# Performance work log

Hardware: AMD Instinct MI355X
Metric: run time of the kernel (lower is better)

## Reference

```python
import jax, jax.numpy as jnp
import numpy as np

N, L, C = 2, 1024, 256
H, E, CL, LAYERS = 64, 16, 64, 4


def setup_inputs() -> dict:
    key = jax.random.key(0)
    ks = jax.random.split(key, 12)
    s = 0.05
    return {
        "x": jax.random.normal(ks[0], (N, L, C), jnp.float32),
        "Wq": jax.random.normal(ks[1], (H * E, C), jnp.float32) * s,
        "bq": jax.random.normal(ks[2], (H * E,), jnp.float32) * s,
        "Wk": jax.random.normal(ks[3], (H * E, C), jnp.float32) * s,
        "bk": jax.random.normal(ks[4], (H * E,), jnp.float32) * s,
        "Wv": jax.random.normal(ks[5], (H, C), jnp.float32) * s,
        "bv": jax.random.normal(ks[6], (H,), jnp.float32) * s,
        "PE": jax.random.uniform(ks[7], (CL, H, E), jnp.float32),
        "fc_w": jax.random.normal(ks[8], (LAYERS, H, H), jnp.float32) * s,
        "fc_b": jax.random.normal(ks[9], (LAYERS, H), jnp.float32) * s,
        "Wout": jax.random.normal(ks[10], (3, H), jnp.float32) * s,
        "bout": jax.random.normal(ks[11], (3,), jnp.float32) * s,
    }


def reference(x, Wq, bq, Wk, bk, Wv, bv, PE, fc_w, fc_b, Wout, bout):
    n, l, c = x.shape
    cl, h, e_dim = PE.shape
    q = (x @ Wq.T + bq).reshape(n, l, h, e_dim)   # (N,L,H,E)
    k = (x @ Wk.T + bk).reshape(n, l, h, e_dim)   # (N,L,H,E)
    v = x @ Wv.T + bv                             # (N,L,H)
    # sliding-window offsets: row i gathers positions i..i+cl-1
    off = jnp.arange(l - cl)[:, None] + jnp.arange(cl)[None, :]  # (L-cl, cl)
    q_mid = q[:, cl // 2: l - cl // 2]            # (N,L-cl,H,E) center queries
    k_win = k[:, off]                             # (N,L-cl,cl,H,E) gathered keys
    # e_{h,id} = q.k + q.PE  (distributed instead of adding PE to k_win)
    e = (jnp.einsum('nlhe,nldhe->nldh', q_mid, k_win)
         + jnp.einsum('nlhe,dhe->nldh', q_mid, PE))
    a = jax.nn.softmax(e, axis=2)                 # softmax over window offset d
    v_win = v[:, off]                             # (N,L-cl,cl,H)
    out = jnp.einsum('nldh,nldh->nlh', a, v_win)  # weighted sum over d
    out = jax.nn.relu(out)
    for i in range(fc_w.shape[0]):                # 1x1 Conv1d stack == per-pos linear
        out = jax.nn.relu(jnp.einsum('nlh,oh->nlo', out, fc_w[i]) + fc_b[i])
    out = jnp.einsum('nlh,oh->nlo', out, Wout) + bout  # (N,L-cl,3)
    return out
```

## Files before the change

### kernel.cpp

```cpp
#include <hip/hip_runtime.h>


typedef __attribute__((ext_vector_type(8))) __bf16 bf16x8;
typedef __attribute__((ext_vector_type(8))) short short8;
typedef __attribute__((ext_vector_type(4))) float f32x4;

__device__ inline unsigned short bf16_rne(float x) {
    unsigned u = __builtin_bit_cast(unsigned, x);
    unsigned r = u + 0x7fffu + ((u >> 16) & 1u);
    return (unsigned short)(r >> 16);
}
__device__ inline float bf16_f(unsigned short h) {
    return __builtin_bit_cast(float, (unsigned)h << 16);
}

__global__ __launch_bounds__(256) void convert_split(
    const float* __restrict__ X,
    const float* __restrict__ Wq, const float* __restrict__ Wk, const float* __restrict__ Wv,
    unsigned short* __restrict__ XhG, unsigned short* __restrict__ XlG,
    unsigned short* __restrict__ WhG, unsigned short* __restrict__ WlG)
{
    const int g = blockIdx.x * 256 + threadIdx.x;
    const int NX = 131072;
    const int NW = 135168;
    if (g >= NX + NW) return;

    float4 v;
    unsigned short *dh, *dl;
    int off;
    if (g < NX) {
        off = g * 4;
        v = *reinterpret_cast<const float4*>(&X[off]);
        dh = XhG; dl = XlG;
    } else {
        off = (g - NX) * 4;
        const int row = off >> 8, col = off & 255;
        const float* s;
        if (row < 1024)      s = &Wq[row * 256 + col];
        else if (row < 2048) s = &Wk[(row - 1024) * 256 + col];
        else                 s = &Wv[(row - 2048) * 256 + col];
        v = *reinterpret_cast<const float4*>(s);
        dh = WhG; dl = WlG;
    }
    unsigned short h0 = bf16_rne(v.x), h1 = bf16_rne(v.y), h2 = bf16_rne(v.z), h3 = bf16_rne(v.w);
    unsigned short l0 = bf16_rne(v.x - bf16_f(h0));
    unsigned short l1 = bf16_rne(v.y - bf16_f(h1));
    unsigned short l2 = bf16_rne(v.z - bf16_f(h2));
    unsigned short l3 = bf16_rne(v.w - bf16_f(h3));
    ushort4 hv = make_ushort4(h0, h1, h2, h3);
    ushort4 lv = make_ushort4(l0, l1, l2, l3);
    *reinterpret_cast<ushort4*>(&dh[off]) = hv;
    *reinterpret_cast<ushort4*>(&dl[off]) = lv;
}

#define LDA 72

__global__ __launch_bounds__(256) void qkv_mfma(
    const unsigned short* __restrict__ XhG, const unsigned short* __restrict__ XlG,
    const unsigned short* __restrict__ WhG, const unsigned short* __restrict__ WlG,
    const float* __restrict__ bq, const float* __restrict__ bk, const float* __restrict__ bv,
    float* __restrict__ qT, float* __restrict__ kT, float* __restrict__ vT)
{
    __shared__ unsigned short A_lds[128 * LDA];
    __shared__ unsigned short B_lds[128 * LDA];
    __shared__ unsigned short C_lds[128 * LDA];

    const int tid = threadIdx.x;
    const int lane = tid & 63;
    const int wid = tid >> 6;
    const int wm = wid >> 1, wn = wid & 1;
    const int m0 = blockIdx.x * 128;
    const int o0 = blockIdx.y * 128;

    f32x4 acc[4][4];
    #pragma unroll
    for (int i = 0; i < 4; ++i)
        #pragma unroll
        for (int j = 0; j < 4; ++j)
            acc[i][j] = f32x4{0.f, 0.f, 0.f, 0.f};

    const short8 zero8 = {0, 0, 0, 0, 0, 0, 0, 0};

    for (int k0 = 0; k0 < 256; k0 += 64) {
        __syncthreads();
        #pragma unroll
        for (int i = tid; i < 1024; i += 256) {
            const int row = i >> 3, lc = (i & 7) * 8;
            *reinterpret_cast<short8*>(&A_lds[row * LDA + lc]) =
                *reinterpret_cast<const short8*>(&XhG[(m0 + row) * 256 + k0 + lc]);
            const int orow = o0 + row;
            short8 wh = zero8, wl = zero8;
            if (orow < 2112) {
                wh = *reinterpret_cast<const short8*>(&WhG[orow * 256 + k0 + lc]);
                wl = *reinterpret_cast<const short8*>(&WlG[orow * 256 + k0 + lc]);
            }
            *reinterpret_cast<short8*>(&B_lds[row * LDA + lc]) = wh;
            *reinterpret_cast<short8*>(&C_lds[row * LDA + lc]) = wl;
        }
        __syncthreads();
        #pragma unroll
        for (int kk = 0; kk < 64; kk += 32) {
            const int colb = kk + ((lane >> 4) << 3);
            bf16x8 aH[4], bH[4], bL[4];
            #pragma unroll
            for (int t = 0; t < 4; ++t) {
                const int ar = wm * 64 + t * 16 + (lane & 15);
                const int br = wn * 64 + t * 16 + (lane & 15);
                aH[t] = __builtin_bit_cast(bf16x8, *reinterpret_cast<const short8*>(&A_lds[ar * LDA + colb]));
                bH[t] = __builtin_bit_cast(bf16x8, *reinterpret_cast<const short8*>(&B_lds[br * LDA + colb]));
                bL[t] = __builtin_bit_cast(bf16x8, *reinterpret_cast<const short8*>(&C_lds[br * LDA + colb]));
            }
            #pragma unroll
            for (int mt = 0; mt < 4; ++mt)
                #pragma unroll
                for (int ot = 0; ot < 4; ++ot) {
                    acc[mt][ot] = __builtin_amdgcn_mfma_f32_16x16x32_bf16(aH[mt], bH[ot], acc[mt][ot], 0, 0, 0);
                    acc[mt][ot] = __builtin_amdgcn_mfma_f32_16x16x32_bf16(aH[mt], bL[ot], acc[mt][ot], 0, 0, 0);
                }
        }
        __syncthreads();
        #pragma unroll
        for (int i = tid; i < 1024; i += 256) {
            const int row = i >> 3, lc = (i & 7) * 8;
            *reinterpret_cast<short8*>(&C_lds[row * LDA + lc]) =
                *reinterpret_cast<const short8*>(&XlG[(m0 + row) * 256 + k0 + lc]);
        }
        __syncthreads();
        #pragma unroll
        for (int kk = 0; kk < 64; kk += 32) {
            const int colb = kk + ((lane >> 4) << 3);
            bf16x8 aL[4], bH[4];
            #pragma unroll
            for (int t = 0; t < 4; ++t) {
                const int ar = wm * 64 + t * 16 + (lane & 15);
                const int br = wn * 64 + t * 16 + (lane & 15);
                aL[t] = __builtin_bit_cast(bf16x8, *reinterpret_cast<const short8*>(&C_lds[ar * LDA + colb]));
                bH[t] = __builtin_bit_cast(bf16x8, *reinterpret_cast<const short8*>(&B_lds[br * LDA + colb]));
            }
            #pragma unroll
            for (int mt = 0; mt < 4; ++mt)
                #pragma unroll
                for (int ot = 0; ot < 4; ++ot)
                    acc[mt][ot] = __builtin_amdgcn_mfma_f32_16x16x32_bf16(aL[mt], bH[ot], acc[mt][ot], 0, 0, 0);
        }
    }

    const int drow = (lane >> 4) * 4;
    const int dcol = lane & 15;
    const int mode = (o0 < 1024) ? 0 : (o0 < 2048 ? 1 : 2);

    if (mode < 2) {
        float* __restrict__ T = mode ? kT : qT;
        const float* __restrict__ bias = mode ? bk : bq;
        const int ob = mode * 1024;
        #pragma unroll
        for (int ot = 0; ot < 4; ++ot) {
            const int o = o0 + wn * 64 + ot * 16 + dcol;
            const int h = (o >> 4) & 63;
            const int e = o & 15;
            const float bval = bias[o - ob];
            #pragma unroll
            for (int mt = 0; mt < 4; ++mt)
                #pragma unroll
                for (int r = 0; r < 4; ++r) {
                    const int m = m0 + wm * 64 + mt * 16 + drow + r;
                    const int n = m >> 10, l = m & 1023;
                    T[((n * 64 + h) * 1024 + l) * 16 + e] = acc[mt][ot][r] + bval;
                }
        }
    } else if (wn == 0) {
        #pragma unroll
        for (int ot = 0; ot < 4; ++ot) {
            const int hV = ot * 16 + dcol;
            const float bval = bv[hV];
            #pragma unroll
            for (int mt = 0; mt < 4; ++mt)
                #pragma unroll
                for (int r = 0; r < 4; ++r) {
                    const int m = m0 + wm * 64 + mt * 16 + drow + r;
                    const int n = m >> 10, l = m & 1023;
                    vT[(n * 64 + hV) * 1024 + l] = acc[mt][ot][r] + bval;
                }
        }
    }
}

__global__ __launch_bounds__(64) void attn_kernel(
    const float* __restrict__ qT, const float* __restrict__ kT,
    const float* __restrict__ vT, const float* __restrict__ PE,
    float* __restrict__ attT)
{
    __shared__ float k_lds[127 * 20];
    __shared__ float pe_lds[64 * 16];
    __shared__ float v_lds[128];

    const int lane = threadIdx.x;
    const int lt = blockIdx.x;
    const int h  = blockIdx.y;
    const int n  = blockIdx.z;
    const int l0 = lt * 64;

    const float4* kb4 = reinterpret_cast<const float4*>(kT + ((size_t)(n * 64 + h) * 1024 + l0) * 16);
    for (int u = lane; u < 508; u += 64) {
        float4 g = kb4[u];
        const int row = u >> 2, f = u & 3;
        *reinterpret_cast<float4*>(&k_lds[row * 20 + f * 4]) = g;
    }
    for (int u = lane; u < 256; u += 64) {
        const int d = u >> 2, f = u & 3;
        *reinterpret_cast<float4*>(&pe_lds[d * 16 + f * 4]) =
            *reinterpret_cast<const float4*>(&PE[(d * 64 + h) * 16 + f * 4]);
    }
    const float* vbase = vT + (size_t)(n * 64 + h) * 1024 + l0;
    for (int u = lane; u < 127; u += 64) v_lds[u] = vbase[u];

    float4 q0, q1, q2, q3;
    {
        const float4* qb = reinterpret_cast<const float4*>(
            qT + ((size_t)(n * 64 + h) * 1024 + l0 + 32 + lane) * 16);
        q0 = qb[0]; q1 = qb[1]; q2 = qb[2]; q3 = qb[3];
    }
    __syncthreads();

    float den = 0.f, pv = 0.f;
    #pragma unroll 2
    for (int d = 0; d < 64; ++d) {
        const float4* kr = reinterpret_cast<const float4*>(&k_lds[(lane + d) * 20]);
        const float4* pr = reinterpret_cast<const float4*>(&pe_lds[d * 16]);
        const float4 k0 = kr[0], k1 = kr[1], k2 = kr[2], k3 = kr[3];
        const float4 p0 = pr[0], p1 = pr[1], p2 = pr[2], p3 = pr[3];
        float s0 = (k0.x + p0.x) * q0.x + (k0.y + p0.y) * q0.y
                 + (k0.z + p0.z) * q0.z + (k0.w + p0.w) * q0.w;
        float s1 = (k1.x + p1.x) * q1.x + (k1.y + p1.y) * q1.y
                 + (k1.z + p1.z) * q1.z + (k1.w + p1.w) * q1.w;
        float s2 = (k2.x + p2.x) * q2.x + (k2.y + p2.y) * q2.y
                 + (k2.z + p2.z) * q2.z + (k2.w + p2.w) * q2.w;
        float s3 = (k3.x + p3.x) * q3.x + (k3.y + p3.y) * q3.y
                 + (k3.z + p3.z) * q3.z + (k3.w + p3.w) * q3.w;
        const float s = (s0 + s1) + (s2 + s3);
        const float p = __expf(s - 16.f);
        den += p;
        pv += p * v_lds[lane + d];
    }
    attT[(size_t)(n * 64 + h) * 960 + l0 + lane] = fmaxf(pv / den, 0.f);
}

__global__ __launch_bounds__(256) void fc_kernel(
    const float* __restrict__ attT,
    const float* __restrict__ fc_w, const float* __restrict__ fc_b,
    const float* __restrict__ Wout, const float* __restrict__ bout,
    float* __restrict__ out)
{
    __shared__ float w_lds[64 * 68];
    __shared__ float wo_lds[3 * 64];
    __shared__ float bufA[4 * 68];
    __shared__ float bufB[4 * 68];

    const int tid = threadIdx.x;
    const int o = tid & 63;
    const int r = tid >> 6;
    const int R0 = blockIdx.x * 4;
    const int n = R0 / 960;
    const int l0 = R0 - n * 960;

    for (int idx = tid; idx < 192; idx += 256) wo_lds[idx] = Wout[idx];
    {
        const int hh = tid >> 2, rr = tid & 3;
        bufA[rr * 68 + hh] = attT[(size_t)(n * 64 + hh) * 960 + l0 + rr];
    }

    float* cur = bufA;
    float* nxt = bufB;

    for (int layer = 0; layer < 4; ++layer) {
        __syncthreads();
        const float4* wsrc = reinterpret_cast<const float4*>(fc_w + layer * 4096);
        for (int u = tid; u < 1024; u += 256) {
            const int oo = u >> 4, f = u & 15;
            *reinterpret_cast<float4*>(&w_lds[oo * 68 + f * 4]) = wsrc[u];
        }
        __syncthreads();
        float acc = fc_b[layer * 64 + o];
        const float4* wr = reinterpret_cast<const float4*>(&w_lds[o * 68]);
        const float4* cr = reinterpret_cast<const float4*>(&cur[r * 68]);
        #pragma unroll
        for (int t = 0; t < 16; ++t) {
            const float4 c = cr[t], w = wr[t];
            acc += c.x * w.x + c.y * w.y + c.z * w.z + c.w * w.w;
        }
        nxt[r * 68 + o] = fmaxf(acc, 0.f);
        float* tmp = cur; cur = nxt; nxt = tmp;
    }
    __syncthreads();

    if (o < 3) {
        float acc = bout[o];
        #pragma unroll
        for (int hh = 0; hh < 64; ++hh)
            acc += cur[r * 68 + hh] * wo_lds[o * 64 + hh];
        out[(R0 + r) * 3 + o] = acc;
    }
}

extern "C" void kernel_launch(void* const* d_in, const int* in_sizes, int n_in,
                              void* d_out, int out_size, void* d_ws, size_t ws_size,
                              hipStream_t stream) {
    const float* x    = (const float*)d_in[0];
    const float* Wq   = (const float*)d_in[1];
    const float* bq   = (const float*)d_in[2];
    const float* Wk   = (const float*)d_in[3];
    const float* bk   = (const float*)d_in[4];
    const float* Wv   = (const float*)d_in[5];
    const float* bv   = (const float*)d_in[6];
    const float* PE   = (const float*)d_in[7];
    const float* fc_w = (const float*)d_in[8];
    const float* fc_b = (const float*)d_in[9];
    const float* Wout = (const float*)d_in[10];
    const float* bout = (const float*)d_in[11];
    float* out = (float*)d_out;

    float* ws = (float*)d_ws;
    float* qT   = ws;
    float* kT   = qT + 2097152;
    float* vT   = kT + 2097152;
    float* attT = vT + 131072;
    unsigned short* XhG = (unsigned short*)(attT + 122880);
    unsigned short* XlG = XhG + 524288;
    unsigned short* WhG = XlG + 524288;
    unsigned short* WlG = WhG + 540672;

    convert_split<<<1040, 256, 0, stream>>>(x, Wq, Wk, Wv, XhG, XlG, WhG, WlG);
    qkv_mfma<<<dim3(16, 17), 256, 0, stream>>>(XhG, XlG, WhG, WlG, bq, bk, bv, qT, kT, vT);
    attn_kernel<<<dim3(15, 64, 2), 64, 0, stream>>>(qT, kT, vT, PE, attT);
    fc_kernel<<<480, 256, 0, stream>>>(attT, fc_w, fc_b, Wout, bout, out);
}
```

Before: 62.59 us.

## Stage QKV GEMM tiles via direct global-to-LDS loads with XOR swizzle

Rewrites the QKV split-bf16 GEMM staging. All four operand tiles (X hi/lo, W hi/lo) are loaded in one pass with global_load_lds straight into an XOR-swizzled LDS buffer, replacing register-staged padded copies and the second reload of X-lo. The block grows to 512 threads (8 waves, each 64x32), and the three MFMAs per tile pair run in a single loop. The intent is to cut LDS staging overhead and barriers and raise the number of waves in flight. The row guard on W was removed, so the last column block reads past the weight rows (into WlG and possibly past it), though those outputs are discarded.

After: 53.00 us. 1.18x faster.

```diff
diff --git a/kernel.cpp b/kernel.cpp
--- a/kernel.cpp
+++ b/kernel.cpp
@@ -53,96 +53,82 @@
     *reinterpret_cast<ushort4*>(&dl[off]) = lv;
 }
 
-#define LDA 72
-
-__global__ __launch_bounds__(256) void qkv_mfma(
+__device__ __forceinline__ bf16x8 ldsfrag(const unsigned short* lds, int t, int row, int so) {
+    return __builtin_bit_cast(bf16x8, *reinterpret_cast<const short8*>(
+        lds + t * 8192 + row * 64 + (((so ^ (row & 7)) & 7) << 3)));
+}
+
+__global__ __launch_bounds__(512, 4) void qkv_mfma(
     const unsigned short* __restrict__ XhG, const unsigned short* __restrict__ XlG,
     const unsigned short* __restrict__ WhG, const unsigned short* __restrict__ WlG,
     const float* __restrict__ bq, const float* __restrict__ bk, const float* __restrict__ bv,
     float* __restrict__ qT, float* __restrict__ kT, float* __restrict__ vT)
 {
-    __shared__ unsigned short A_lds[128 * LDA];
-    __shared__ unsigned short B_lds[128 * LDA];
-    __shared__ unsigned short C_lds[128 * LDA];
-
-    const int tid = threadIdx.x;
+    __shared__ unsigned short lds[4 * 128 * 64];
+
+    const int tid  = threadIdx.x;
     const int lane = tid & 63;
-    const int wid = tid >> 6;
-    const int wm = wid >> 1, wn = wid & 1;
+    const int wid  = tid >> 6;
+    const int wm   = wid >> 2;
+    const int wn   = wid & 3;
     const int m0 = blockIdx.x * 128;
     const int o0 = blockIdx.y * 128;
 
-    f32x4 acc[4][4];
+    f32x4 acc[4][2];
     #pragma unroll
     for (int i = 0; i < 4; ++i)
         #pragma unroll
-        for (int j = 0; j < 4; ++j)
+        for (int j = 0; j < 2; ++j)
             acc[i][j] = f32x4{0.f, 0.f, 0.f, 0.f};
 
-    const short8 zero8 = {0, 0, 0, 0, 0, 0, 0, 0};
+    const int r8 = lane >> 3;
+    const int ss = (lane & 7) ^ r8;
 
     for (int k0 = 0; k0 < 256; k0 += 64) {
+        #pragma unroll
+        for (int j = 0; j < 8; ++j) {
+            const int c   = (wid << 3) | j;
+            const int t   = c >> 4;
+            const int rg  = c & 15;
+            const int row = (rg << 3) + r8;
+            const unsigned short* gsrc;
+            if (t == 0)      gsrc = &XhG[(m0 + row) * 256 + k0 + (ss << 3)];
+            else if (t == 1) gsrc = &XlG[(m0 + row) * 256 + k0 + (ss << 3)];
+            else if (t == 2) gsrc = &WhG[(o0 + row) * 256 + k0 + (ss << 3)];
+            else             gsrc = &WlG[(o0 + row) * 256 + k0 + (ss << 3)];
+            char* lbase = (char*)lds + (c << 10);
+            __builtin_amdgcn_global_load_lds(
+                (const __attribute__((address_space(1))) void*)gsrc,
+                (__attribute__((address_space(3))) void*)lbase, 16, 0, 0);
+        }
         __syncthreads();
-        #pragma unroll
-        for (int i = tid; i < 1024; i += 256) {
-            const int row = i >> 3, lc = (i & 7) * 8;
-            *reinterpret_cast<short8*>(&A_lds[row * LDA + lc]) =
-                *reinterpret_cast<const short8*>(&XhG[(m0 + row) * 256 + k0 + lc]);
-            const int orow = o0 + row;
-            short8 wh = zero8, wl = zero8;
-            if (orow < 2112) {
-                wh = *reinterpret_cast<const short8*>(&WhG[orow * 256 + k0 + lc]);
-                wl = *reinterpret_cast<const short8*>(&WlG[orow * 256 + k0 + lc]);
+
+        #pragma unroll
+        for (int kk = 0; kk < 64; kk += 32) {
+            const int so = (kk >> 3) + (lane >> 4);
+            bf16x8 aH[4], aL[4], bH[2], bL[2];
+            #pragma unroll
+            for (int mt = 0; mt < 4; ++mt) {
+                const int ar = wm * 64 + mt * 16 + (lane & 15);
+                aH[mt] = ldsfrag(lds, 0, ar, so);
+                aL[mt] = ldsfrag(lds, 1, ar, so);
             }
-            *reinterpret_cast<short8*>(&B_lds[row * LDA + lc]) = wh;
-            *reinterpret_cast<short8*>(&C_lds[row * LDA + lc]) = wl;
-        }
-        __syncthreads();
-        #pragma unroll
-        for (int kk = 0; kk < 64; kk += 32) {
-            const int colb = kk + ((lane >> 4) << 3);
-            bf16x8 aH[4], bH[4], bL[4];
-            #pragma unroll
-            for (int t = 0; t < 4; ++t) {
-                const int ar = wm * 64 + t * 16 + (lane & 15);
-                const int br = wn * 64 + t * 16 + (lane & 15);
-                aH[t] = __builtin_bit_cast(bf16x8, *reinterpret_cast<const short8*>(&A_lds[ar * LDA + colb]));
-                bH[t] = __builtin_bit_cast(bf16x8, *reinterpret_cast<const short8*>(&B_lds[br * LDA + colb]));
-                bL[t] = __builtin_bit_cast(bf16x8, *reinterpret_cast<const short8*>(&C_lds[br * LDA + colb]));
+            #pragma unroll
+            for (int ot = 0; ot < 2; ++ot) {
+                const int br = wn * 32 + ot * 16 + (lane & 15);
+                bH[ot] = ldsfrag(lds, 2, br, so);
+                bL[ot] = ldsfrag(lds, 3, br, so);
             }
             #pragma unroll
             for (int mt = 0; mt < 4; ++mt)
                 #pragma unroll
-                for (int ot = 0; ot < 4; ++ot) {
+                for (int ot = 0; ot < 2; ++ot) {
                     acc[mt][ot] = __builtin_amdgcn_mfma_f32_16x16x32_bf16(aH[mt], bH[ot], acc[mt][ot], 0, 0, 0);
                     acc[mt][ot] = __builtin_amdgcn_mfma_f32_16x16x32_bf16(aH[mt], bL[ot], acc[mt][ot], 0, 0, 0);
+                    acc[mt][ot] = __builtin_amdgcn_mfma_f32_16x16x32_bf16(aL[mt], bH[ot], acc[mt][ot], 0, 0, 0);
                 }
         }
         __syncthreads();
-        #pragma unroll
-        for (int i = tid; i < 1024; i += 256) {
-            const int row = i >> 3, lc = (i & 7) * 8;
-            *reinterpret_cast<short8*>(&C_lds[row * LDA + lc]) =
-                *reinterpret_cast<const short8*>(&XlG[(m0 + row) * 256 + k0 + lc]);
-        }
-        __syncthreads();
-        #pragma unroll
-        for (int kk = 0; kk < 64; kk += 32) {
-            const int colb = kk + ((lane >> 4) << 3);
-            bf16x8 aL[4], bH[4];
-            #pragma unroll
-            for (int t = 0; t < 4; ++t) {
-                const int ar = wm * 64 + t * 16 + (lane & 15);
-                const int br = wn * 64 + t * 16 + (lane & 15);
-                aL[t] = __builtin_bit_cast(bf16x8, *reinterpret_cast<const short8*>(&C_lds[ar * LDA + colb]));
-                bH[t] = __builtin_bit_cast(bf16x8, *reinterpret_cast<const short8*>(&B_lds[br * LDA + colb]));
-            }
-            #pragma unroll
-            for (int mt = 0; mt < 4; ++mt)
-                #pragma unroll
-                for (int ot = 0; ot < 4; ++ot)
-                    acc[mt][ot] = __builtin_amdgcn_mfma_f32_16x16x32_bf16(aL[mt], bH[ot], acc[mt][ot], 0, 0, 0);
-        }
     }
 
     const int drow = (lane >> 4) * 4;
@@ -154,8 +140,8 @@
         const float* __restrict__ bias = mode ? bk : bq;
         const int ob = mode * 1024;
         #pragma unroll
-        for (int ot = 0; ot < 4; ++ot) {
-            const int o = o0 + wn * 64 + ot * 16 + dcol;
+        for (int ot = 0; ot < 2; ++ot) {
+            const int o = o0 + wn * 32 + ot * 16 + dcol;
             const int h = (o >> 4) & 63;
             const int e = o & 15;
             const float bval = bias[o - ob];
@@ -168,10 +154,10 @@
                     T[((n * 64 + h) * 1024 + l) * 16 + e] = acc[mt][ot][r] + bval;
                 }
         }
-    } else if (wn == 0) {
-        #pragma unroll
-        for (int ot = 0; ot < 4; ++ot) {
-            const int hV = ot * 16 + dcol;
+    } else if (wn < 2) {
+        #pragma unroll
+        for (int ot = 0; ot < 2; ++ot) {
+            const int hV = wn * 32 + ot * 16 + dcol;
             const float bval = bv[hV];
             #pragma unroll
             for (int mt = 0; mt < 4; ++mt)
@@ -330,7 +316,7 @@
     unsigned short* WlG = WhG + 540672;
 
     convert_split<<<1040, 256, 0, stream>>>(x, Wq, Wk, Wv, XhG, XlG, WhG, WlG);
-    qkv_mfma<<<dim3(16, 17), 256, 0, stream>>>(XhG, XlG, WhG, WlG, bq, bk, bv, qT, kT, vT);
+    qkv_mfma<<<dim3(16, 17), 512, 0, stream>>>(XhG, XlG, WhG, WlG, bq, bk, bv, qT, kT, vT);
     attn_kernel<<<dim3(15, 64, 2), 64, 0, stream>>>(qT, kT, vT, PE, attT);
     fc_kernel<<<480, 256, 0, stream>>>(attT, fc_w, fc_b, Wout, bout, out);
 }
```
